# Kernel tuning notes

Hardware: AMD Instinct MI355X
Metric: run time of the kernel (lower is better)

## Reference

```python
import jax, jax.numpy as jnp
import numpy as np

BETA = 6.0
LOG_2PI = float(np.log(2.0 * np.pi))


def setup_inputs() -> dict:
    key = jax.random.key(0)
    k1, k2, k3, k4 = jax.random.split(key, 4)
    B, L = 2048, 64
    kl = jax.random.uniform(k1, (B, L), dtype=jnp.float32)
    z_mean = jax.random.normal(k2, (B, L), dtype=jnp.float32)
    z_logvar = jax.random.normal(k3, (B, L), dtype=jnp.float32)
    z_sampled = jax.random.normal(k4, (B, L), dtype=jnp.float32)
    return {"kl": kl, "z_mean": z_mean, "z_logvar": z_logvar, "z_sampled": z_sampled}


def gaussian_log_density(samples, mean, log_var):
    # samples: [B,1,L], mean/log_var: [1,B,L] -> [B,B,L]
    tmp = samples - mean
    return -0.5 * (tmp * tmp * jnp.exp(-log_var) + log_var + LOG_2PI)


def total_correlation(z, z_mean, z_logvar):
    # [B, B, L]: log q(z_i_l | x_j)
    log_qz_prob = gaussian_log_density(z[:, None, :], z_mean[None, :, :], z_logvar[None, :, :])
    # sum_l logsumexp_j -> [B]
    log_qz_product = jnp.sum(jax.scipy.special.logsumexp(log_qz_prob, axis=1), axis=1)
    # logsumexp_j sum_l -> [B]
    log_qz = jax.scipy.special.logsumexp(jnp.sum(log_qz_prob, axis=2), axis=1)
    return jnp.mean(log_qz - log_qz_product)


def reference(kl, z_mean, z_logvar, z_sampled):
    kl_loss = jnp.sum(kl)
    tc = (BETA - 1.0) * total_correlation(z_sampled, z_mean, z_logvar)
    return tc + kl_loss
```

## Files before the change

kernel.cpp:

```cpp
#include <hip/hip_runtime.h>
#include <math.h>


#define NB 2048
#define NL 64
#define NE (NB * NL)
#define BVAL 12.0f

typedef float v2f __attribute__((ext_vector_type(2)));

__device__ __forceinline__ v2f fma2(v2f a, v2f b, v2f c) {
#if __has_builtin(__builtin_elementwise_fma)
  return __builtin_elementwise_fma(a, b, c);
#else
  v2f r;
  r.x = fmaf(a.x, b.x, c.x);
  r.y = fmaf(a.y, b.y, c.y);
  return r;
#endif
}

__device__ __forceinline__ float wredsum(float v) {
#pragma unroll
  for (int o = 32; o; o >>= 1) v += __shfl_xor(v, o, 64);
  return v;
}
__device__ __forceinline__ float wredmax(float v) {
#pragma unroll
  for (int o = 32; o; o >>= 1) v = fmaxf(v, __shfl_xor(v, o, 64));
  return v;
}

__global__ __launch_bounds__(256) void ka_pre(const float* __restrict__ kl,
                                              const float* __restrict__ zm,
                                              const float* __restrict__ zlv,
                                              float4* __restrict__ PK2,
                                              float* __restrict__ A2T,
                                              float* __restrict__ MA2T,
                                              float* __restrict__ QC2,
                                              float* __restrict__ KLP,
                                              int* __restrict__ CNT) {
  const float INVLN2 = 1.4426950408889634f;
  const float LOG2PI = 1.8378770664093453f;
  int tid = threadIdx.x;
  int e = blockIdx.x * 256 + tid;
  int j = e >> 6, l = e & 63;
  float lv = zlv[e], m = zm[e];
  float a2 = -0.5f * INVLN2 * __expf(-lv);
  float b2 = -0.5f * INVLN2 * (lv + LOG2PI);
  float c1 = -2.0f * a2 * m;
  float c0 = fmaf(a2 * m, m, b2);
  PK2[e] = make_float4(a2, c1, c0 - BVAL, 0.0f);
  A2T[l * NB + j] = a2;
  MA2T[l * NB + j] = c1;
  float q = wredsum(c0);
  if (l == 0) QC2[j] = q;
  float ks = wredsum(kl[e]);
  __shared__ float sk[4];
  if (l == 0) sk[tid >> 6] = ks;
  __syncthreads();
  if (tid == 0) KLP[blockIdx.x] = sk[0] + sk[1] + sk[2] + sk[3];
  if (blockIdx.x == 0 && tid == 0) *CNT = 0;
}

__global__ __launch_bounds__(256) void k2_t(const float* __restrict__ zs,
                                            const float* __restrict__ A2T,
                                            const float* __restrict__ MA2T,
                                            const float* __restrict__ QC2,
                                            float* __restrict__ TPM,
                                            float* __restrict__ TPS) {
  int jc = blockIdx.x;
  int i0 = blockIdx.y * 8;
  int tid = threadIdx.x;
  int w = tid >> 6;
  int j = jc * 256 + tid;
  __shared__ float zsh[64][8];
  if (tid < 128) {
    int k = tid >> 1, r0 = (tid & 1) * 4;
#pragma unroll
    for (int r = 0; r < 4; ++r) zsh[k][r0 + r] = zs[(i0 + r0 + r) * NL + k];
  }
  __syncthreads();
  float accv[8];
  float q = QC2[j];
#pragma unroll
  for (int r = 0; r < 8; ++r) accv[r] = q;
  for (int k = 0; k < 64; ++k) {
    float av = A2T[k * NB + j];
    float mv = MA2T[k * NB + j];
    const float4* z4 = (const float4*)&zsh[k][0];
    float4 za = z4[0], zb = z4[1];
    float zk[8] = {za.x, za.y, za.z, za.w, zb.x, zb.y, zb.z, zb.w};
#pragma unroll
    for (int r = 0; r < 8; ++r) {
      accv[r] = fmaf(zk[r] * zk[r], av, accv[r]);
      accv[r] = fmaf(zk[r], mv, accv[r]);
    }
  }
  __shared__ float lm[4][8], ls[4][8];
#pragma unroll
  for (int r = 0; r < 8; ++r) {
    float mx = wredmax(accv[r]);
    if ((tid & 63) == 0) lm[w][r] = mx;
  }
  __syncthreads();
  float Mt[8];
#pragma unroll
  for (int r = 0; r < 8; ++r)
    Mt[r] = fmaxf(fmaxf(lm[0][r], lm[1][r]), fmaxf(lm[2][r], lm[3][r]));
#pragma unroll
  for (int r = 0; r < 8; ++r) {
    float ss = wredsum(__builtin_amdgcn_exp2f(accv[r] - Mt[r]));
    if ((tid & 63) == 0) ls[w][r] = ss;
  }
  __syncthreads();
  if (tid == 0) {
#pragma unroll
    for (int r = 0; r < 8; ++r) {
      TPM[(i0 + r) * 8 + jc] = Mt[r];
      TPS[(i0 + r) * 8 + jc] = ls[0][r] + ls[1][r] + ls[2][r] + ls[3][r];
    }
  }
}

__global__ __launch_bounds__(256) void k3_lse(const float* __restrict__ zs,
                                              const float4* __restrict__ PK2,
                                              float* __restrict__ SP) {
  int jc = blockIdx.x;
  int i0 = blockIdx.y * 16;
  int tid = threadIdx.x;
  int w = tid >> 6, l = tid & 63;
  const float4* p = PK2 + (size_t)(jc * 128 + w * 32) * NL + l;
  v2f zr[8];
#pragma unroll
  for (int r = 0; r < 8; ++r) {
    zr[r].x = zs[(i0 + 2 * r) * NL + l];
    zr[r].y = zs[(i0 + 2 * r + 1) * NL + l];
  }
  v2f S[8];
#pragma unroll
  for (int r = 0; r < 8; ++r) S[r] = (v2f){0.0f, 0.0f};
#pragma unroll 2
  for (int jj = 0; jj < 32; ++jj) {
    float4 c = p[(size_t)jj * NL];
    v2f ca = (v2f){c.x, c.x}, cb = (v2f){c.y, c.y}, cc = (v2f){c.z, c.z};
#pragma unroll
    for (int r = 0; r < 8; ++r) {
      v2f t = fma2(zr[r], ca, cb);
      v2f lp = fma2(t, zr[r], cc);
      v2f e;
      e.x = __builtin_amdgcn_exp2f(lp.x);
      e.y = __builtin_amdgcn_exp2f(lp.y);
      S[r] += e;
    }
  }
  float* sp = SP + (size_t)(jc * 4 + w) * NE;
#pragma unroll
  for (int r = 0; r < 8; ++r) {
    sp[(size_t)(i0 + 2 * r) * NL + l] = S[r].x;
    sp[(size_t)(i0 + 2 * r + 1) * NL + l] = S[r].y;
  }
}

__global__ __launch_bounds__(256) void kc_fin(const float* __restrict__ SP,
                                              const float* __restrict__ TPM,
                                              const float* __restrict__ TPS,
                                              const float* __restrict__ KLP,
                                              float* __restrict__ PERB,
                                              int* __restrict__ CNT,
                                              float* __restrict__ out) {
  int tid = threadIdx.x;
  int w = tid >> 6, l = tid & 63;
  int i = blockIdx.x * 4 + w;
  float S = 0.0f;
#pragma unroll 8
  for (int s = 0; s < 64; ++s) S += SP[(size_t)s * NE + (size_t)i * NL + l];
  float val = __builtin_amdgcn_logf(S);
  float lqp2 = wredsum(val) + 64.0f * BVAL;
  float tm = (l < 8) ? TPM[i * 8 + l] : -1e30f;
  float ts = (l < 8) ? TPS[i * 8 + l] : 0.0f;
  float Mt = wredmax(tm);
  float St = wredsum(ts * __builtin_amdgcn_exp2f(tm - Mt));
  float lqz2 = Mt + __builtin_amdgcn_logf(St);
  __shared__ float sblk[4];
  if (l == 0) sblk[w] = lqz2 - lqp2;
  __syncthreads();
  __shared__ int slast;
  if (tid == 0) {
    float v = sblk[0] + sblk[1] + sblk[2] + sblk[3];
    __hip_atomic_store(&PERB[blockIdx.x], v, __ATOMIC_RELEASE, __HIP_MEMORY_SCOPE_AGENT);
    int old = __hip_atomic_fetch_add(CNT, 1, __ATOMIC_ACQ_REL, __HIP_MEMORY_SCOPE_AGENT);
    slast = (old == 511) ? 1 : 0;
  }
  __syncthreads();
  if (!slast) return;
  float a = 0.0f, b = 0.0f;
  for (int x = tid; x < 512; x += 256) {
    a += KLP[x];
    b += __hip_atomic_load(&PERB[x], __ATOMIC_ACQUIRE, __HIP_MEMORY_SCOPE_AGENT);
  }
  float ra = wredsum(a), rb = wredsum(b);
  __shared__ float sa[4], sb[4];
  if (l == 0) {
    sa[w] = ra;
    sb[w] = rb;
  }
  __syncthreads();
  if (tid == 0) {
    const float LN2 = 0.6931471805599453f;
    float ka = sa[0] + sa[1] + sa[2] + sa[3];
    float kb = sb[0] + sb[1] + sb[2] + sb[3];
    out[0] = ka + 5.0f * LN2 * kb * (1.0f / (float)NB);
  }
}

extern "C" void kernel_launch(void* const* d_in, const int* in_sizes, int n_in,
                              void* d_out, int out_size, void* d_ws, size_t ws_size,
                              hipStream_t stream) {
  const float* kl = (const float*)d_in[0];
  const float* zm = (const float*)d_in[1];
  const float* zlv = (const float*)d_in[2];
  const float* zs = (const float*)d_in[3];
  float* ws = (float*)d_ws;

  float* PK2 = ws;
  float* A2T = PK2 + 4 * NE;
  float* MA2T = A2T + NE;
  float* QC2 = MA2T + NE;
  float* SP = QC2 + NB;
  float* TPM = SP + 64 * (size_t)NE;
  float* TPS = TPM + NB * 8;
  float* KLP = TPS + NB * 8;
  float* PERB = KLP + 512;
  int* CNT = (int*)(PERB + 512);

  ka_pre<<<NE / 256, 256, 0, stream>>>(kl, zm, zlv, (float4*)PK2, A2T, MA2T, QC2,
                                       KLP, CNT);
  k2_t<<<dim3(8, NB / 8), 256, 0, stream>>>(zs, A2T, MA2T, QC2, TPM, TPS);
  k3_lse<<<dim3(16, NB / 16), 256, 0, stream>>>(zs, (const float4*)PK2, SP);
  kc_fin<<<512, 256, 0, stream>>>(SP, TPM, TPS, KLP, PERB, CNT, (float*)d_out);
}
```

Before: 149.0 us.

## Replace exp2 with bit-trick float-to-int conversion and enlarge k3 tiles with LDS reduction

```diff
diff --git a/kernel.cpp b/kernel.cpp
--- a/kernel.cpp
+++ b/kernel.cpp
@@ -6,6 +6,8 @@
 #define NL 64
 #define NE (NB * NL)
 #define BVAL 12.0f
+#define EXP_SCALE 8388608.0f
+#define EXP_MAGIC 1064866805.0f
 
 typedef float v2f __attribute__((ext_vector_type(2)));
 
@@ -18,6 +20,12 @@
   r.y = fmaf(a.y, b.y, c.y);
   return r;
 #endif
+}
+
+__device__ __forceinline__ float exp2_fast_tail(float p) {
+  unsigned u;
+  asm("v_cvt_u32_f32 %0, %1" : "=v"(u) : "v"(p));
+  return __builtin_bit_cast(float, u);
 }
 
 __device__ __forceinline__ float wredsum(float v) {
@@ -50,7 +58,8 @@
   float b2 = -0.5f * INVLN2 * (lv + LOG2PI);
   float c1 = -2.0f * a2 * m;
   float c0 = fmaf(a2 * m, m, b2);
-  PK2[e] = make_float4(a2, c1, c0 - BVAL, 0.0f);
+  PK2[e] = make_float4(a2 * EXP_SCALE, c1 * EXP_SCALE,
+                       fmaf(c0 - BVAL, EXP_SCALE, EXP_MAGIC), 0.0f);
   A2T[l * NB + j] = a2;
   MA2T[l * NB + j] = c1;
   float q = wredsum(c0);
@@ -127,38 +136,44 @@
                                               const float4* __restrict__ PK2,
                                               float* __restrict__ SP) {
   int jc = blockIdx.x;
-  int i0 = blockIdx.y * 16;
+  int i0 = blockIdx.y * 32;
   int tid = threadIdx.x;
   int w = tid >> 6, l = tid & 63;
-  const float4* p = PK2 + (size_t)(jc * 128 + w * 32) * NL + l;
-  v2f zr[8];
-#pragma unroll
-  for (int r = 0; r < 8; ++r) {
+  const float4* p = PK2 + (size_t)(jc * 256 + w * 64) * NL + l;
+  v2f zr[16];
+#pragma unroll
+  for (int r = 0; r < 16; ++r) {
     zr[r].x = zs[(i0 + 2 * r) * NL + l];
     zr[r].y = zs[(i0 + 2 * r + 1) * NL + l];
   }
-  v2f S[8];
-#pragma unroll
-  for (int r = 0; r < 8; ++r) S[r] = (v2f){0.0f, 0.0f};
+  v2f S[16];
+#pragma unroll
+  for (int r = 0; r < 16; ++r) S[r] = (v2f){0.0f, 0.0f};
 #pragma unroll 2
-  for (int jj = 0; jj < 32; ++jj) {
+  for (int jj = 0; jj < 64; ++jj) {
     float4 c = p[(size_t)jj * NL];
     v2f ca = (v2f){c.x, c.x}, cb = (v2f){c.y, c.y}, cc = (v2f){c.z, c.z};
 #pragma unroll
-    for (int r = 0; r < 8; ++r) {
+    for (int r = 0; r < 16; ++r) {
       v2f t = fma2(zr[r], ca, cb);
-      v2f lp = fma2(t, zr[r], cc);
+      v2f pa = fma2(t, zr[r], cc);
       v2f e;
-      e.x = __builtin_amdgcn_exp2f(lp.x);
-      e.y = __builtin_amdgcn_exp2f(lp.y);
+      e.x = exp2_fast_tail(pa.x);
+      e.y = exp2_fast_tail(pa.y);
       S[r] += e;
     }
   }
-  float* sp = SP + (size_t)(jc * 4 + w) * NE;
-#pragma unroll
-  for (int r = 0; r < 8; ++r) {
-    sp[(size_t)(i0 + 2 * r) * NL + l] = S[r].x;
-    sp[(size_t)(i0 + 2 * r + 1) * NL + l] = S[r].y;
+  __shared__ float lss[4][32][64];
+#pragma unroll
+  for (int r = 0; r < 16; ++r) {
+    lss[w][2 * r][l] = S[r].x;
+    lss[w][2 * r + 1][l] = S[r].y;
+  }
+  __syncthreads();
+  for (int pp = tid; pp < 2048; pp += 256) {
+    int ii = pp >> 6, ll = pp & 63;
+    float Sc = lss[0][ii][ll] + lss[1][ii][ll] + lss[2][ii][ll] + lss[3][ii][ll];
+    SP[(size_t)jc * NE + (size_t)(i0 + ii) * NL + ll] = Sc;
   }
 }
 
@@ -173,8 +188,8 @@
   int w = tid >> 6, l = tid & 63;
   int i = blockIdx.x * 4 + w;
   float S = 0.0f;
-#pragma unroll 8
-  for (int s = 0; s < 64; ++s) S += SP[(size_t)s * NE + (size_t)i * NL + l];
+#pragma unroll
+  for (int s = 0; s < 8; ++s) S += SP[(size_t)s * NE + (size_t)i * NL + l];
   float val = __builtin_amdgcn_logf(S);
   float lqp2 = wredsum(val) + 64.0f * BVAL;
   float tm = (l < 8) ? TPM[i * 8 + l] : -1e30f;
@@ -228,7 +243,7 @@
   float* MA2T = A2T + NE;
   float* QC2 = MA2T + NE;
   float* SP = QC2 + NB;
-  float* TPM = SP + 64 * (size_t)NE;
+  float* TPM = SP + 8 * NE;
   float* TPS = TPM + NB * 8;
   float* KLP = TPS + NB * 8;
   float* PERB = KLP + 512;
@@ -237,6 +252,6 @@
   ka_pre<<<NE / 256, 256, 0, stream>>>(kl, zm, zlv, (float4*)PK2, A2T, MA2T, QC2,
                                        KLP, CNT);
   k2_t<<<dim3(8, NB / 8), 256, 0, stream>>>(zs, A2T, MA2T, QC2, TPM, TPS);
-  k3_lse<<<dim3(16, NB / 16), 256, 0, stream>>>(zs, (const float4*)PK2, SP);
+  k3_lse<<<dim3(8, NB / 32), 256, 0, stream>>>(zs, (const float4*)PK2, SP);
   kc_fin<<<512, 256, 0, stream>>>(SP, TPM, TPS, KLP, PERB, CNT, (float*)d_out);
 }
```

Measured after the change: 141.2 us. 1.06x faster.
